# Performance work log

Hardware: AMD Instinct MI355X
Metric: run time of the kernel (lower is better)

Reference implementation:

```python
import jax, jax.numpy as jnp
import numpy as np


def _per_qubit_unitary(theta):
    # theta: [L, Nq, 3] float -> combined per-qubit 2x2 unitary [Nq, 2, 2] complex64
    # Circuit applies, for each layer l (l=0 first): RZ(theta[l,i,0]) -> RY(theta[l,i,1]) -> RZ(theta[l,i,2])
    half = theta.astype(jnp.float32) * 0.5

    def rz(p):  # p: [Nq] -> [Nq,2,2]
        e = jnp.exp(-1j * p)  # complex64
        z = jnp.zeros_like(e)
        return jnp.stack([jnp.stack([e, z], -1), jnp.stack([z, jnp.conj(e)], -1)], -2)

    def ry(p):  # p: [Nq] -> [Nq,2,2]
        c, s = jnp.cos(p), jnp.sin(p)
        return jnp.stack([jnp.stack([c, -s], -1), jnp.stack([s, c], -1)], -2).astype(jnp.complex64)

    n_layers, n_qubits = theta.shape[0], theta.shape[1]
    U = jnp.broadcast_to(jnp.eye(2, dtype=jnp.complex64), (n_qubits, 2, 2))
    for l in range(n_layers):  # small fixed layer loop
        Ul = rz(half[l, :, 2]) @ ry(half[l, :, 1]) @ rz(half[l, :, 0])
        U = Ul @ U
    return U


def _vqc_state(angles, theta):
    # angles: [B,S,Nq]; theta: [L,Nq,3] -> real part of 2^Nq state vector, [B,S,2^Nq]
    half = angles * 0.5
    # RY(a)|0> = cos(a/2)|0> + sin(a/2)|1>
    v = jnp.stack([jnp.cos(half), jnp.sin(half)], -1).astype(jnp.complex64)  # [B,S,Nq,2]
    U = _per_qubit_unitary(theta)  # [Nq,2,2]
    v = jnp.einsum('nij,bsnj->bsni', U, v)  # apply layered single-qubit unitaries
    # Kron across qubits; PennyLane wire 0 is most significant -> left-to-right kron
    state = v[:, :, 0, :]  # [B,S,2]
    n_qubits = v.shape[2]
    for q in range(1, n_qubits):  # small fixed qubit loop
        state = (state[..., :, None] * v[:, :, q][..., None, :])
        state = state.reshape(state.shape[0], state.shape[1], -1)
    return jnp.real(state)


def setup_inputs() -> dict:
    key = jax.random.key(0)
    k0, k1, k2, k3 = jax.random.split(key, 4)
    B, S, NQ, L = 8, 512, 12, 4
    return {
        'angles': jax.random.normal(k0, (B, S, NQ), dtype=jnp.float32),
        'theta_Q': jax.random.normal(k1, (L, NQ, 3), dtype=jnp.float32),
        'theta_K': jax.random.normal(k2, (L, NQ, 3), dtype=jnp.float32),
        'theta_V': jax.random.normal(k3, (L, NQ, 3), dtype=jnp.float32),
    }


def reference(angles, theta_Q, theta_K, theta_V):
    psi_Q = _vqc_state(angles, theta_Q)
    psi_K = _vqc_state(angles, theta_K)
    psi_V = _vqc_state(angles, theta_V)
    return (psi_Q, psi_K, psi_V)
```

## Files before the change

### kernel.cpp

```cpp
#include <hip/hip_runtime.h>


#define BS_TOTAL 4096
#define NQ 12
#define NL 4
#define NSTATE 4096
#define SPB 2

typedef float vfloat4 __attribute__((ext_vector_type(4)));

__device__ __forceinline__ float2 cmul(float2 a, float2 b) {
    return make_float2(a.x * b.x - a.y * b.y, a.x * b.y + a.y * b.x);
}
__device__ __forceinline__ float2 cconj(float2 a) { return make_float2(a.x, -a.y); }
__device__ __forceinline__ float2 cadd(float2 a, float2 b) { return make_float2(a.x + b.x, a.y + b.y); }

__global__ __launch_bounds__(256) void vqc_fused_kernel(
    const float* __restrict__ angles,
    const float* __restrict__ tQ,
    const float* __restrict__ tK,
    const float* __restrict__ tV,
    float* __restrict__ out)
{
    const int bs0 = blockIdx.x * SPB;
    const int t   = threadIdx.x;

    __shared__ float2 Uu[3][NQ][4];
    __shared__ float  cs[SPB][NQ][2];
    __shared__ float2 vv[SPB][3][NQ][2];
    __shared__ float2 AB[SPB][3][2][16];
    __shared__ float2 Plo[SPB][3][16];
    __shared__ float2 Phi[SPB][3][256];

    if (t < 36) {
        int m = t / NQ, n = t % NQ;
        const float* th = (m == 0) ? tQ : (m == 1) ? tK : tV;
        float2 U00 = {1.f, 0.f}, U01 = {0.f, 0.f}, U10 = {0.f, 0.f}, U11 = {1.f, 0.f};
#pragma unroll
        for (int l = 0; l < NL; ++l) {
            float c = 0.5f * th[(l * NQ + n) * 3 + 0];
            float b = 0.5f * th[(l * NQ + n) * 3 + 1];
            float a = 0.5f * th[(l * NQ + n) * 3 + 2];
            float sa, ca, sb, cb, sc, cc;
            sincosf(a, &sa, &ca);
            sincosf(b, &sb, &cb);
            sincosf(c, &sc, &cc);
            float2 ea = {ca, -sa};
            float2 ec = {cc, -sc};
            float2 p  = cmul(ea, ec);
            float2 q  = cmul(ea, cconj(ec));
            float2 A00 = { cb * p.x,  cb * p.y};
            float2 A01 = {-sb * q.x, -sb * q.y};
            float2 A10 = { sb * q.x, -sb * q.y};
            float2 A11 = { cb * p.x, -cb * p.y};
            float2 n00 = cadd(cmul(A00, U00), cmul(A01, U10));
            float2 n01 = cadd(cmul(A00, U01), cmul(A01, U11));
            float2 n10 = cadd(cmul(A10, U00), cmul(A11, U10));
            float2 n11 = cadd(cmul(A10, U01), cmul(A11, U11));
            U00 = n00; U01 = n01; U10 = n10; U11 = n11;
        }
        Uu[m][n][0] = U00; Uu[m][n][1] = U01; Uu[m][n][2] = U10; Uu[m][n][3] = U11;
    } else if (t >= 64 && t < 64 + SPB * NQ) {
        int idx = t - 64, s2 = idx / NQ, n = idx % NQ;
        float a = angles[(bs0 + s2) * NQ + n];
        float s, c;
        sincosf(0.5f * a, &s, &c);
        cs[s2][n][0] = c; cs[s2][n][1] = s;
    }
    __syncthreads();

    if (t < SPB * 36) {
        int s2 = t / 36, r = t % 36, m = r / NQ, n = r % NQ;
        float c = cs[s2][n][0], s = cs[s2][n][1];
        float2 u00 = Uu[m][n][0], u01 = Uu[m][n][1], u10 = Uu[m][n][2], u11 = Uu[m][n][3];
        vv[s2][m][n][0] = make_float2(u00.x * c + u01.x * s, u00.y * c + u01.y * s);
        vv[s2][m][n][1] = make_float2(u10.x * c + u11.x * s, u10.y * c + u11.y * s);
    }
    __syncthreads();

#pragma unroll
    for (int task = t; task < SPB * 144; task += 256) {
        int s2 = task / 144, r = task % 144, m = r / 48, g = (r % 48) / 16, idx = r % 16;
        int q0 = g * 4;
        float2 p = cmul(cmul(vv[s2][m][q0    ][(idx >> 3) & 1],
                             vv[s2][m][q0 + 1][(idx >> 2) & 1]),
                        cmul(vv[s2][m][q0 + 2][(idx >> 1) & 1],
                             vv[s2][m][q0 + 3][ idx       & 1]));
        if (g < 2) AB[s2][m][g][idx] = p; else Plo[s2][m][idx] = p;
    }
    __syncthreads();

#pragma unroll
    for (int i = 0; i < 6; ++i) {
        int task = t + i * 256;
        int s2 = task / 768, r = task % 768, m = r / 256, e = r % 256;
        Phi[s2][m][e] = cmul(AB[s2][m][0][e >> 4], AB[s2][m][1][e & 15]);
    }
    __syncthreads();

    const int lobase = 4 * (t & 3);
    const int hsub   = t >> 2;
#pragma unroll
    for (int s2 = 0; s2 < SPB; ++s2) {
#pragma unroll
        for (int m = 0; m < 3; ++m) {
            float2 l0 = Plo[s2][m][lobase + 0];
            float2 l1 = Plo[s2][m][lobase + 1];
            float2 l2 = Plo[s2][m][lobase + 2];
            float2 l3 = Plo[s2][m][lobase + 3];
            float* po = out + (size_t)m * BS_TOTAL * NSTATE + (size_t)(bs0 + s2) * NSTATE;
#pragma unroll
            for (int j = 0; j < 4; ++j) {
                float2 h = Phi[s2][m][j * 64 + hsub];
                vfloat4 r;
                r.x = h.x * l0.x - h.y * l0.y;
                r.y = h.x * l1.x - h.y * l1.y;
                r.z = h.x * l2.x - h.y * l2.y;
                r.w = h.x * l3.x - h.y * l3.y;
                __builtin_nontemporal_store(r, (vfloat4*)(po + j * 1024 + t * 4));
            }
        }
    }
}

extern "C" void kernel_launch(void* const* d_in, const int* in_sizes, int n_in,
                              void* d_out, int out_size, void* d_ws, size_t ws_size,
                              hipStream_t stream) {
    (void)in_sizes; (void)n_in; (void)out_size; (void)d_ws; (void)ws_size;
    const float* angles = (const float*)d_in[0];
    const float* tQ     = (const float*)d_in[1];
    const float* tK     = (const float*)d_in[2];
    const float* tV     = (const float*)d_in[3];

    vqc_fused_kernel<<<BS_TOTAL / SPB, 256, 0, stream>>>(angles, tQ, tK, tV, (float*)d_out);
}
```

Measured before the change: 208.5 us.

## Parallelize layer unitaries, drop Phi stage, double samples per block

Per-layer 2x2 matrices are now computed by 144 threads in parallel and then multiplied together by 36 threads. The Phi shared-memory stage and its barrier are removed, and the high-part product is computed inline during the output store. SPB goes from 2 to 4 so each block handles more samples and amortizes the unitary setup. Stores switch from nontemporal vector stores to plain float4 stores, which may change cache behavior on this write-bound kernel.

```diff
diff --git a/kernel.cpp b/kernel.cpp
--- a/kernel.cpp
+++ b/kernel.cpp
@@ -5,9 +5,7 @@
 #define NQ 12
 #define NL 4
 #define NSTATE 4096
-#define SPB 2
-
-typedef float vfloat4 __attribute__((ext_vector_type(4)));
+#define SPB 4
 
 __device__ __forceinline__ float2 cmul(float2 a, float2 b) {
     return make_float2(a.x * b.x - a.y * b.y, a.x * b.y + a.y * b.x);
@@ -25,43 +23,32 @@
     const int bs0 = blockIdx.x * SPB;
     const int t   = threadIdx.x;
 
-    __shared__ float2 Uu[3][NQ][4];
+    __shared__ float2 Lm[36][NL][4];
     __shared__ float  cs[SPB][NQ][2];
     __shared__ float2 vv[SPB][3][NQ][2];
     __shared__ float2 AB[SPB][3][2][16];
     __shared__ float2 Plo[SPB][3][16];
-    __shared__ float2 Phi[SPB][3][256];
 
-    if (t < 36) {
-        int m = t / NQ, n = t % NQ;
+    if (t < 144) {
+        int l = t & 3, mn = t >> 2, m = mn / NQ, n = mn % NQ;
         const float* th = (m == 0) ? tQ : (m == 1) ? tK : tV;
-        float2 U00 = {1.f, 0.f}, U01 = {0.f, 0.f}, U10 = {0.f, 0.f}, U11 = {1.f, 0.f};
-#pragma unroll
-        for (int l = 0; l < NL; ++l) {
-            float c = 0.5f * th[(l * NQ + n) * 3 + 0];
-            float b = 0.5f * th[(l * NQ + n) * 3 + 1];
-            float a = 0.5f * th[(l * NQ + n) * 3 + 2];
-            float sa, ca, sb, cb, sc, cc;
-            sincosf(a, &sa, &ca);
-            sincosf(b, &sb, &cb);
-            sincosf(c, &sc, &cc);
-            float2 ea = {ca, -sa};
-            float2 ec = {cc, -sc};
-            float2 p  = cmul(ea, ec);
-            float2 q  = cmul(ea, cconj(ec));
-            float2 A00 = { cb * p.x,  cb * p.y};
-            float2 A01 = {-sb * q.x, -sb * q.y};
-            float2 A10 = { sb * q.x, -sb * q.y};
-            float2 A11 = { cb * p.x, -cb * p.y};
-            float2 n00 = cadd(cmul(A00, U00), cmul(A01, U10));
-            float2 n01 = cadd(cmul(A00, U01), cmul(A01, U11));
-            float2 n10 = cadd(cmul(A10, U00), cmul(A11, U10));
-            float2 n11 = cadd(cmul(A10, U01), cmul(A11, U11));
-            U00 = n00; U01 = n01; U10 = n10; U11 = n11;
-        }
-        Uu[m][n][0] = U00; Uu[m][n][1] = U01; Uu[m][n][2] = U10; Uu[m][n][3] = U11;
-    } else if (t >= 64 && t < 64 + SPB * NQ) {
-        int idx = t - 64, s2 = idx / NQ, n = idx % NQ;
+        float c = 0.5f * th[(l * NQ + n) * 3 + 0];
+        float b = 0.5f * th[(l * NQ + n) * 3 + 1];
+        float a = 0.5f * th[(l * NQ + n) * 3 + 2];
+        float sa, ca, sb, cb, sc, cc;
+        sincosf(a, &sa, &ca);
+        sincosf(b, &sb, &cb);
+        sincosf(c, &sc, &cc);
+        float2 ea = {ca, -sa};
+        float2 ec = {cc, -sc};
+        float2 p  = cmul(ea, ec);
+        float2 q  = cmul(ea, cconj(ec));
+        Lm[mn][l][0] = make_float2( cb * p.x,  cb * p.y);
+        Lm[mn][l][1] = make_float2(-sb * q.x, -sb * q.y);
+        Lm[mn][l][2] = make_float2( sb * q.x, -sb * q.y);
+        Lm[mn][l][3] = make_float2( cb * p.x, -cb * p.y);
+    } else if (t >= 160 && t < 160 + SPB * NQ) {
+        int idx = t - 160, s2 = idx / NQ, n = idx % NQ;
         float a = angles[(bs0 + s2) * NQ + n];
         float s, c;
         sincosf(0.5f * a, &s, &c);
@@ -69,12 +56,24 @@
     }
     __syncthreads();
 
-    if (t < SPB * 36) {
-        int s2 = t / 36, r = t % 36, m = r / NQ, n = r % NQ;
-        float c = cs[s2][n][0], s = cs[s2][n][1];
-        float2 u00 = Uu[m][n][0], u01 = Uu[m][n][1], u10 = Uu[m][n][2], u11 = Uu[m][n][3];
-        vv[s2][m][n][0] = make_float2(u00.x * c + u01.x * s, u00.y * c + u01.y * s);
-        vv[s2][m][n][1] = make_float2(u10.x * c + u11.x * s, u10.y * c + u11.y * s);
+    if (t < 36) {
+        int m = t / NQ, n = t % NQ;
+        float2 U00 = Lm[t][0][0], U01 = Lm[t][0][1], U10 = Lm[t][0][2], U11 = Lm[t][0][3];
+#pragma unroll
+        for (int l = 1; l < NL; ++l) {
+            float2 A00 = Lm[t][l][0], A01 = Lm[t][l][1], A10 = Lm[t][l][2], A11 = Lm[t][l][3];
+            float2 n00 = cadd(cmul(A00, U00), cmul(A01, U10));
+            float2 n01 = cadd(cmul(A00, U01), cmul(A01, U11));
+            float2 n10 = cadd(cmul(A10, U00), cmul(A11, U10));
+            float2 n11 = cadd(cmul(A10, U01), cmul(A11, U11));
+            U00 = n00; U01 = n01; U10 = n10; U11 = n11;
+        }
+#pragma unroll
+        for (int s2 = 0; s2 < SPB; ++s2) {
+            float c = cs[s2][n][0], s = cs[s2][n][1];
+            vv[s2][m][n][0] = make_float2(U00.x * c + U01.x * s, U00.y * c + U01.y * s);
+            vv[s2][m][n][1] = make_float2(U10.x * c + U11.x * s, U10.y * c + U11.y * s);
+        }
     }
     __syncthreads();
 
@@ -90,14 +89,6 @@
     }
     __syncthreads();
 
-#pragma unroll
-    for (int i = 0; i < 6; ++i) {
-        int task = t + i * 256;
-        int s2 = task / 768, r = task % 768, m = r / 256, e = r % 256;
-        Phi[s2][m][e] = cmul(AB[s2][m][0][e >> 4], AB[s2][m][1][e & 15]);
-    }
-    __syncthreads();
-
     const int lobase = 4 * (t & 3);
     const int hsub   = t >> 2;
 #pragma unroll
@@ -108,16 +99,17 @@
             float2 l1 = Plo[s2][m][lobase + 1];
             float2 l2 = Plo[s2][m][lobase + 2];
             float2 l3 = Plo[s2][m][lobase + 3];
+            float2 b1 = AB[s2][m][1][hsub & 15];
             float* po = out + (size_t)m * BS_TOTAL * NSTATE + (size_t)(bs0 + s2) * NSTATE;
 #pragma unroll
             for (int j = 0; j < 4; ++j) {
-                float2 h = Phi[s2][m][j * 64 + hsub];
-                vfloat4 r;
+                float2 h = cmul(AB[s2][m][0][j * 4 + (hsub >> 4)], b1);
+                float4 r;
                 r.x = h.x * l0.x - h.y * l0.y;
                 r.y = h.x * l1.x - h.y * l1.y;
                 r.z = h.x * l2.x - h.y * l2.y;
                 r.w = h.x * l3.x - h.y * l3.y;
-                __builtin_nontemporal_store(r, (vfloat4*)(po + j * 1024 + t * 4));
+                *(float4*)(po + j * 1024 + t * 4) = r;
             }
         }
     }
```

After: 198.3 us. 4.9% less time.
